# Kernel optimization log

Hardware: AMD Instinct MI355X
Metric: run time of the kernel (lower is better)

The kernel has to match this reference:

```python
import jax, jax.numpy as jnp
import numpy as np

NEG_INF = -1e9  # finite stand-in for torch's masked_fill(-inf); grad-safe


def setup_inputs() -> dict:
    key = jax.random.key(0)
    k1, k2, k3, k4, k5 = jax.random.split(key, 5)
    B, T, S, Dq, Dk = 8, 2048, 4096, 128, 128
    query = jax.random.normal(k1, (B, T, Dq), dtype=jnp.float32)
    memory_bank = jax.random.normal(k2, (B, S, Dk), dtype=jnp.float32)
    # lengths in [1, S] so every row has at least one valid source position
    memory_lengths = jax.random.randint(k3, (B,), 1, S + 1, dtype=jnp.int64)
    # nn.Linear weights: linear_in [Dk, Dq], linear_out [Dq, Dq+Dk]
    W_in = jax.random.normal(k4, (Dk, Dq), dtype=jnp.float32) / np.sqrt(Dq)
    W_out = jax.random.normal(k5, (Dq, Dq + Dk), dtype=jnp.float32) / np.sqrt(Dq + Dk)
    return {"query": query, "memory_bank": memory_bank,
            "memory_lengths": memory_lengths, "W_in": W_in, "W_out": W_out}


def reference(query, memory_bank, memory_lengths, W_in, W_out):
    B, T, Dq = query.shape
    S = memory_bank.shape[1]
    # score: project query then bmm with sources -> [B, T, S]
    h_t = jnp.einsum('btq,kq->btk', query, W_in)
    align = jnp.einsum('btk,bsk->bts', h_t, memory_bank)
    # mask invalid source positions
    valid = jnp.arange(S) < memory_lengths[:, None]            # [B, S]
    align = jnp.where(valid[:, None, :], align, NEG_INF)       # [B, T, S]
    align_vectors = jax.nn.softmax(align, axis=-1)
    # context and output projection
    c = jnp.einsum('bts,bsk->btk', align_vectors, memory_bank)  # [B, T, Dk]
    concat_c = jnp.concatenate([c, query], axis=-1)             # [B, T, Dk+Dq]
    attn_h = jnp.tanh(jnp.einsum('btc,qc->btq', concat_c, W_out))
    return attn_h, align_vectors, align
```

## Files before the change

kernel.cpp:

```cpp
#include <hip/hip_runtime.h>

#define B_ 8
#define T_ 2048
#define S_ 4096
#define D_ 128
#define N_ (B_*T_)
#define NTILE_ (S_/128)
#define NEG_INF_ (-1e9f)

__device__ __forceinline__ int load_len(const int* __restrict__ p, int b) {
    return (p[1] == 0) ? p[2*b] : p[b];
}

template<bool MASK>
__global__ __launch_bounds__(256) void gemm_nt_k128(
    const float* __restrict__ A, const float* __restrict__ Bmat,
    float* __restrict__ C, const int ldc, const long long bStride,
    const int* __restrict__ mlen,
    float* __restrict__ pmax, float* __restrict__ psum)
{
    __shared__ float At[16][128];
    __shared__ float Bt[16][128];
    const int t  = threadIdx.x;
    const int tx = t & 15, ty = t >> 4;
    const int col0 = blockIdx.x << 7;
    const int n0   = blockIdx.y << 7;
    const int b    = blockIdx.y >> 4;
    const float* Bb = Bmat + (long long)b * bStride;
    const int r_ld = t >> 1, kf = t & 1;

    float acc[8][8];
#pragma unroll
    for (int i = 0; i < 8; ++i)
#pragma unroll
        for (int j = 0; j < 8; ++j) acc[i][j] = 0.f;

    const float* Arow = &A[(long long)(n0 + r_ld) * 128];
    const float* Brow = &Bb[(long long)(col0 + r_ld) * 128];

    for (int k0 = 0; k0 < 128; k0 += 16) {
        __syncthreads();
#pragma unroll
        for (int u = 0; u < 2; ++u) {
            const int kk = kf*8 + u*4;
            const float4 va = *(const float4*)&Arow[k0 + kk];
            At[kk+0][r_ld] = va.x; At[kk+1][r_ld] = va.y;
            At[kk+2][r_ld] = va.z; At[kk+3][r_ld] = va.w;
            const float4 vb = *(const float4*)&Brow[k0 + kk];
            Bt[kk+0][r_ld] = vb.x; Bt[kk+1][r_ld] = vb.y;
            Bt[kk+2][r_ld] = vb.z; Bt[kk+3][r_ld] = vb.w;
        }
        __syncthreads();
#pragma unroll
        for (int kk = 0; kk < 16; ++kk) {
            float a[8], bv[8];
#pragma unroll
            for (int u = 0; u < 2; ++u) {
                const float4 v = *(const float4*)&At[kk][ty*8 + u*4];
                a[u*4+0]=v.x; a[u*4+1]=v.y; a[u*4+2]=v.z; a[u*4+3]=v.w;
                const float4 w = *(const float4*)&Bt[kk][tx*4 + u*64];
                bv[u*4+0]=w.x; bv[u*4+1]=w.y; bv[u*4+2]=w.z; bv[u*4+3]=w.w;
            }
#pragma unroll
            for (int i = 0; i < 8; ++i)
#pragma unroll
                for (int j = 0; j < 8; ++j)
                    acc[i][j] = fmaf(a[i], bv[j], acc[i][j]);
        }
    }

    if (MASK) {
        const int len = load_len(mlen, b);
#pragma unroll
        for (int i = 0; i < 8; ++i) {
            const int row = n0 + ty*8 + i;
            float* Crow = &C[(long long)row * ldc + col0];
            float m = -3.4e38f;
#pragma unroll
            for (int j = 0; j < 8; ++j) {
                const int cl = tx*4 + (j&3) + ((j>>2)<<6);
                float v = acc[i][j];
                if (col0 + cl >= len) v = NEG_INF_;
                acc[i][j] = v;
                m = fmaxf(m, v);
            }
            float4 w0, w1;
            w0.x=acc[i][0]; w0.y=acc[i][1]; w0.z=acc[i][2]; w0.w=acc[i][3];
            w1.x=acc[i][4]; w1.y=acc[i][5]; w1.z=acc[i][6]; w1.w=acc[i][7];
            *(float4*)&Crow[tx*4]      = w0;
            *(float4*)&Crow[tx*4 + 64] = w1;
#pragma unroll
            for (int off = 1; off < 16; off <<= 1) m = fmaxf(m, __shfl_xor(m, off, 64));
            float s = 0.f;
#pragma unroll
            for (int j = 0; j < 8; ++j) s += __expf(acc[i][j] - m);
#pragma unroll
            for (int off = 1; off < 16; off <<= 1) s += __shfl_xor(s, off, 64);
            if (tx == 0) {
                pmax[(long long)blockIdx.x * N_ + row] = m;
                psum[(long long)blockIdx.x * N_ + row] = s;
            }
        }
    } else {
#pragma unroll
        for (int i = 0; i < 8; ++i) {
            float* Crow = &C[(long long)(n0 + ty*8 + i) * ldc + col0];
            float4 w0, w1;
            w0.x=acc[i][0]; w0.y=acc[i][1]; w0.z=acc[i][2]; w0.w=acc[i][3];
            w1.x=acc[i][4]; w1.y=acc[i][5]; w1.z=acc[i][6]; w1.w=acc[i][7];
            *(float4*)&Crow[tx*4]      = w0;
            *(float4*)&Crow[tx*4 + 64] = w1;
        }
    }
}

__global__ __launch_bounds__(256) void merge_stats(
    const float* __restrict__ pmax, const float* __restrict__ psum,
    float* __restrict__ rmax, float* __restrict__ rrinv)
{
    const int r = blockIdx.x * 256 + threadIdx.x;
    float pm[NTILE_];
    float M = -3.4e38f;
#pragma unroll
    for (int i = 0; i < NTILE_; ++i) {
        pm[i] = pmax[(long long)i * N_ + r];
        M = fmaxf(M, pm[i]);
    }
    float S = 0.f;
#pragma unroll
    for (int i = 0; i < NTILE_; ++i)
        S += psum[(long long)i * N_ + r] * __expf(pm[i] - M);
    rmax[r]  = M;
    rrinv[r] = 1.0f / S;
}

__global__ __launch_bounds__(256) void av_cpart(
    const float* __restrict__ al, const float* __restrict__ mb,
    const float* __restrict__ rmax, const float* __restrict__ rrinv,
    float* __restrict__ av, float* __restrict__ cpart, const int sChunks)
{
    __shared__ float Pl[32][132];
    __shared__ float Ml[32][132];
    const int n0 = blockIdx.y << 7;
    const int b  = blockIdx.y >> 4;
    const int t  = threadIdx.x;
    const int tx = t & 15, ty = t >> 4;
    const int r_ld = t >> 1, sf = t & 1;
    const int s_m  = t >> 3, kq8 = t & 7;

    const float mM = rmax[n0 + r_ld];
    const float rR = rrinv[n0 + r_ld];

    float acc[8][8];
#pragma unroll
    for (int i = 0; i < 8; ++i)
#pragma unroll
        for (int j = 0; j < 8; ++j) acc[i][j] = 0.f;

    const int ch0 = blockIdx.x * sChunks;
    for (int ch = 0; ch < sChunks; ++ch) {
        const int s0 = (ch0 + ch) << 5;
        __syncthreads();
#pragma unroll
        for (int f = 0; f < 4; ++f) {
            const int sl = sf*16 + f*4;
            const long long g = (long long)(n0 + r_ld) * S_ + s0 + sl;
            const float4 vv = *(const float4*)&al[g];
            float4 p;
            p.x = __expf(vv.x - mM) * rR;
            p.y = __expf(vv.y - mM) * rR;
            p.z = __expf(vv.z - mM) * rR;
            p.w = __expf(vv.w - mM) * rR;
            *(float4*)&av[g] = p;
            Pl[sl+0][r_ld] = p.x; Pl[sl+1][r_ld] = p.y;
            Pl[sl+2][r_ld] = p.z; Pl[sl+3][r_ld] = p.w;
        }
#pragma unroll
        for (int f = 0; f < 4; ++f) {
            const int k = kq8*16 + f*4;
            *(float4*)&Ml[s_m][k] =
                *(const float4*)&mb[((long long)b*S_ + s0 + s_m)*128 + k];
        }
        __syncthreads();
#pragma unroll 2
        for (int s = 0; s < 32; ++s) {
            float a[8], bv[8];
#pragma unroll
            for (int u = 0; u < 2; ++u) {
                const float4 v = *(const float4*)&Pl[s][ty*8 + u*4];
                a[u*4+0]=v.x; a[u*4+1]=v.y; a[u*4+2]=v.z; a[u*4+3]=v.w;
                const float4 w = *(const float4*)&Ml[s][tx*4 + u*64];
                bv[u*4+0]=w.x; bv[u*4+1]=w.y; bv[u*4+2]=w.z; bv[u*4+3]=w.w;
            }
#pragma unroll
            for (int i = 0; i < 8; ++i)
#pragma unroll
                for (int j = 0; j < 8; ++j)
                    acc[i][j] = fmaf(a[i], bv[j], acc[i][j]);
        }
    }

    float* cp = cpart + (long long)blockIdx.x * N_ * 128;
#pragma unroll
    for (int i = 0; i < 8; ++i) {
        const long long ro = (long long)(n0 + ty*8 + i) * 128;
        float4 w0, w1;
        w0.x=acc[i][0]; w0.y=acc[i][1]; w0.z=acc[i][2]; w0.w=acc[i][3];
        w1.x=acc[i][4]; w1.y=acc[i][5]; w1.z=acc[i][6]; w1.w=acc[i][7];
        *(float4*)&cp[ro + tx*4]      = w0;
        *(float4*)&cp[ro + tx*4 + 64] = w1;
    }
}

__global__ __launch_bounds__(256) void combine_proj(
    const float* __restrict__ cpart, const int nSplit,
    const float* __restrict__ query, const float* __restrict__ Wout,
    float* __restrict__ attn)
{
    __shared__ float Cl[32][132];
    __shared__ float Ql[32][132];
    const int n0 = blockIdx.x << 5;
    const int t = threadIdx.x;
    const int r = t >> 3, kq = t & 7;
#pragma unroll
    for (int f = 0; f < 4; ++f) {
        const int k = kq*16 + f*4;
        const long long idx = (long long)(n0 + r) * 128 + k;
        float4 s4 = *(const float4*)&cpart[idx];
        for (int p = 1; p < nSplit; ++p) {
            const float4 v = *(const float4*)&cpart[(long long)p * N_ * 128 + idx];
            s4.x += v.x; s4.y += v.y; s4.z += v.z; s4.w += v.w;
        }
        *(float4*)&Cl[r][k] = s4;
        *(float4*)&Ql[r][k] = *(const float4*)&query[idx];
    }
    __syncthreads();

    const int j = t & 127, rh = t >> 7;
    float acc2[16];
#pragma unroll
    for (int rr = 0; rr < 16; ++rr) acc2[rr] = 0.f;
    const float4* Wrow = (const float4*)&Wout[j * 256];

    for (int k4 = 0; k4 < 32; ++k4) {
        const float4 w = Wrow[k4];
#pragma unroll
        for (int rr = 0; rr < 16; ++rr) {
            const float4 c4 = *(const float4*)&Cl[rh*16 + rr][k4*4];
            acc2[rr] = fmaf(c4.x, w.x, fmaf(c4.y, w.y, fmaf(c4.z, w.z, fmaf(c4.w, w.w, acc2[rr]))));
        }
    }
    for (int k4 = 0; k4 < 32; ++k4) {
        const float4 w = Wrow[32 + k4];
#pragma unroll
        for (int rr = 0; rr < 16; ++rr) {
            const float4 q4 = *(const float4*)&Ql[rh*16 + rr][k4*4];
            acc2[rr] = fmaf(q4.x, w.x, fmaf(q4.y, w.y, fmaf(q4.z, w.z, fmaf(q4.w, w.w, acc2[rr]))));
        }
    }
#pragma unroll
    for (int rr = 0; rr < 16; ++rr)
        attn[(long long)(n0 + rh*16 + rr) * 128 + j] = tanhf(acc2[rr]);
}

extern "C" void kernel_launch(void* const* d_in, const int* in_sizes, int n_in,
                              void* d_out, int out_size, void* d_ws, size_t ws_size,
                              hipStream_t stream)
{
    const float* query = (const float*)d_in[0];
    const float* mb    = (const float*)d_in[1];
    const int*   mlen  = (const int*)d_in[2];
    const float* Win   = (const float*)d_in[3];
    const float* Wout  = (const float*)d_in[4];

    float* attn  = (float*)d_out;
    float* av    = attn + (size_t)N_ * D_;
    float* align = av   + (size_t)N_ * S_;

    const size_t statsB = (size_t)2 * N_ * 4;
    const size_t partB  = (size_t)2 * NTILE_ * N_ * 4;
    const size_t matB   = (size_t)N_ * D_ * 4;

    int split = 0;
    if      (ws_size >= statsB + partB + matB + 8*matB) split = 8;
    else if (ws_size >= statsB + partB + matB + 4*matB) split = 4;
    else if (ws_size >= statsB + partB + matB + 2*matB) split = 2;
    else if (ws_size >= statsB + partB + matB + 1*matB) split = 1;

    char* w = (char*)d_ws;
    float* rmax  = (float*)w;
    float* rrinv = rmax + N_;
    float *pmax, *psum, *cpart, *ht;
    int nSplit;
    if (split > 0) {
        pmax  = (float*)(w + statsB);
        psum  = pmax + (size_t)NTILE_ * N_;
        cpart = (float*)(w + statsB + partB);
        ht    = cpart + (size_t)split * N_ * D_;
        nSplit = split;
    } else {
        pmax  = av;
        psum  = av + (size_t)NTILE_ * N_;
        ht    = av + (size_t)2 * NTILE_ * N_;
        cpart = attn;
        nSplit = 1;
    }

    gemm_nt_k128<false><<<dim3(1, 128), 256, 0, stream>>>(
        query, Win, ht, 128, 0LL, nullptr, nullptr, nullptr);
    gemm_nt_k128<true><<<dim3(S_/128, 128), 256, 0, stream>>>(
        ht, mb, align, S_, (long long)S_ * D_, mlen, pmax, psum);
    merge_stats<<<N_/256, 256, 0, stream>>>(pmax, psum, rmax, rrinv);
    av_cpart<<<dim3(nSplit, 128), 256, 0, stream>>>(
        align, mb, rmax, rrinv, av, cpart, (S_/32) / nSplit);
    combine_proj<<<N_/32, 256, 0, stream>>>(cpart, nSplit, query, Wout, attn);
}
```

Baseline: 965.9 us.

## Use split-bf16 MFMA for score and context GEMMs with masked-tile skipping

Replaces the FP32 SIMT GEMMs for align and context with bf16 MFMA kernels. Each FP32 operand is split into hi and lo bf16 parts and three MFMAs are issued per product to keep near-FP32 accuracy. It adds preprocessing kernels that split and transpose memory_bank and h_t, and it skips compute for tiles and chunks beyond memory_lengths by writing the mask or zero values directly. The cost is extra workspace and conversion traffic, plus a small precision change from dropping the lo*lo term.

```diff
diff --git a/kernel.cpp b/kernel.cpp
--- a/kernel.cpp
+++ b/kernel.cpp
@@ -8,25 +8,76 @@
 #define NTILE_ (S_/128)
 #define NEG_INF_ (-1e9f)
 
+typedef __attribute__((ext_vector_type(8))) short bf16x8;
+typedef __attribute__((ext_vector_type(4))) float f32x4;
+
 __device__ __forceinline__ int load_len(const int* __restrict__ p, int b) {
     return (p[1] == 0) ? p[2*b] : p[b];
 }
 
-template<bool MASK>
-__global__ __launch_bounds__(256) void gemm_nt_k128(
+__device__ __forceinline__ unsigned short f2bf(float x) {
+    unsigned u = __float_as_uint(x);
+    unsigned r = (u + 0x7fffu + ((u >> 16) & 1u)) >> 16;
+    return (unsigned short)r;
+}
+__device__ __forceinline__ float bf2f(unsigned short h) {
+    return __uint_as_float(((unsigned)h) << 16);
+}
+__device__ __forceinline__ unsigned pk2(unsigned short a, unsigned short b) {
+    return (unsigned)a | ((unsigned)b << 16);
+}
+
+__global__ __launch_bounds__(256) void prep_mb(
+    const float* __restrict__ mb,
+    unsigned short* __restrict__ mbh, unsigned short* __restrict__ mbl,
+    unsigned short* __restrict__ mbth, unsigned short* __restrict__ mbtl)
+{
+    __shared__ float tile[64][65];
+    const int b = blockIdx.z, f0 = blockIdx.y << 6, s0 = blockIdx.x << 6;
+    const int t = threadIdx.x;
+#pragma unroll
+    for (int i = 0; i < 4; ++i) {
+        const int c = t + (i << 8);
+        const int s = c >> 4, q = c & 15;
+        const long long ga = ((long long)(b*S_ + s0 + s)) * 128 + f0 + q*4;
+        const float4 v = *(const float4*)&mb[ga];
+        tile[s][q*4+0] = v.x; tile[s][q*4+1] = v.y;
+        tile[s][q*4+2] = v.z; tile[s][q*4+3] = v.w;
+        unsigned short h0=f2bf(v.x), h1=f2bf(v.y), h2=f2bf(v.z), h3=f2bf(v.w);
+        uint2 ph; ph.x = pk2(h0,h1); ph.y = pk2(h2,h3);
+        *(uint2*)&mbh[ga] = ph;
+        uint2 pl; pl.x = pk2(f2bf(v.x - bf2f(h0)), f2bf(v.y - bf2f(h1)));
+        pl.y = pk2(f2bf(v.z - bf2f(h2)), f2bf(v.w - bf2f(h3)));
+        *(uint2*)&mbl[ga] = pl;
+    }
+    __syncthreads();
+    const int f = t >> 2, q = t & 3;
+    unsigned short h[16], l[16];
+#pragma unroll
+    for (int ss = 0; ss < 16; ++ss) {
+        const float v = tile[q*16 + ss][f];
+        h[ss] = f2bf(v);
+        l[ss] = f2bf(v - bf2f(h[ss]));
+    }
+    const long long go = ((long long)(b*128 + f0 + f)) * S_ + s0 + q*16;
+    uint4 w0, w1;
+    w0.x=pk2(h[0],h[1]);  w0.y=pk2(h[2],h[3]);  w0.z=pk2(h[4],h[5]);  w0.w=pk2(h[6],h[7]);
+    w1.x=pk2(h[8],h[9]);  w1.y=pk2(h[10],h[11]);w1.z=pk2(h[12],h[13]);w1.w=pk2(h[14],h[15]);
+    *(uint4*)&mbth[go] = w0; *(uint4*)&mbth[go+8] = w1;
+    w0.x=pk2(l[0],l[1]);  w0.y=pk2(l[2],l[3]);  w0.z=pk2(l[4],l[5]);  w0.w=pk2(l[6],l[7]);
+    w1.x=pk2(l[8],l[9]);  w1.y=pk2(l[10],l[11]);w1.z=pk2(l[12],l[13]);w1.w=pk2(l[14],l[15]);
+    *(uint4*)&mbtl[go] = w0; *(uint4*)&mbtl[go+8] = w1;
+}
+
+__global__ __launch_bounds__(256) void ht_gemm(
     const float* __restrict__ A, const float* __restrict__ Bmat,
-    float* __restrict__ C, const int ldc, const long long bStride,
-    const int* __restrict__ mlen,
-    float* __restrict__ pmax, float* __restrict__ psum)
+    float* __restrict__ C)
 {
     __shared__ float At[16][128];
     __shared__ float Bt[16][128];
     const int t  = threadIdx.x;
     const int tx = t & 15, ty = t >> 4;
-    const int col0 = blockIdx.x << 7;
-    const int n0   = blockIdx.y << 7;
-    const int b    = blockIdx.y >> 4;
-    const float* Bb = Bmat + (long long)b * bStride;
+    const int n0 = blockIdx.y << 7;
     const int r_ld = t >> 1, kf = t & 1;
 
     float acc[8][8];
@@ -36,7 +87,7 @@
         for (int j = 0; j < 8; ++j) acc[i][j] = 0.f;
 
     const float* Arow = &A[(long long)(n0 + r_ld) * 128];
-    const float* Brow = &Bb[(long long)(col0 + r_ld) * 128];
+    const float* Brow = &Bmat[(long long)r_ld * 128];
 
     for (int k0 = 0; k0 < 128; k0 += 16) {
         __syncthreads();
@@ -68,49 +119,155 @@
                     acc[i][j] = fmaf(a[i], bv[j], acc[i][j]);
         }
     }
-
-    if (MASK) {
-        const int len = load_len(mlen, b);
-#pragma unroll
-        for (int i = 0; i < 8; ++i) {
-            const int row = n0 + ty*8 + i;
-            float* Crow = &C[(long long)row * ldc + col0];
-            float m = -3.4e38f;
-#pragma unroll
-            for (int j = 0; j < 8; ++j) {
-                const int cl = tx*4 + (j&3) + ((j>>2)<<6);
-                float v = acc[i][j];
-                if (col0 + cl >= len) v = NEG_INF_;
-                acc[i][j] = v;
-                m = fmaxf(m, v);
+#pragma unroll
+    for (int i = 0; i < 8; ++i) {
+        float* Crow = &C[(long long)(n0 + ty*8 + i) * 128];
+        float4 w0, w1;
+        w0.x=acc[i][0]; w0.y=acc[i][1]; w0.z=acc[i][2]; w0.w=acc[i][3];
+        w1.x=acc[i][4]; w1.y=acc[i][5]; w1.z=acc[i][6]; w1.w=acc[i][7];
+        *(float4*)&Crow[tx*4]      = w0;
+        *(float4*)&Crow[tx*4 + 64] = w1;
+    }
+}
+
+__global__ __launch_bounds__(256) void split_bf16(
+    const float* __restrict__ in, unsigned short* __restrict__ hi,
+    unsigned short* __restrict__ lo, int n4)
+{
+    const int i = blockIdx.x * 256 + threadIdx.x;
+    if (i >= n4) return;
+    const float4 v = *(const float4*)&in[i*4];
+    unsigned short h0=f2bf(v.x), h1=f2bf(v.y), h2=f2bf(v.z), h3=f2bf(v.w);
+    uint2 ph; ph.x = pk2(h0,h1); ph.y = pk2(h2,h3);
+    *(uint2*)&hi[i*4] = ph;
+    uint2 pl; pl.x = pk2(f2bf(v.x-bf2f(h0)), f2bf(v.y-bf2f(h1)));
+    pl.y = pk2(f2bf(v.z-bf2f(h2)), f2bf(v.w-bf2f(h3)));
+    *(uint2*)&lo[i*4] = pl;
+}
+
+__global__ __launch_bounds__(256) void qk_mfma(
+    const unsigned short* __restrict__ hth, const unsigned short* __restrict__ htl,
+    const unsigned short* __restrict__ mbh, const unsigned short* __restrict__ mbl,
+    float* __restrict__ alignO, const int* __restrict__ mlen,
+    float* __restrict__ pmax, float* __restrict__ psum)
+{
+    __shared__ __align__(16) unsigned short Ah[128*40], Al[128*40];
+    __shared__ __align__(16) unsigned short Bh[128*40], Bl[128*40];
+    __shared__ float sm[2][128], ss[2][128];
+    const int t = threadIdx.x, l = t & 63, w = t >> 6;
+    const int wm = w >> 1, wn = w & 1, g = l >> 4, lr = l & 15;
+    const int c0 = blockIdx.x << 7, n0 = blockIdx.y << 7;
+    const int b  = blockIdx.y >> 4;
+    const int len = load_len(mlen, b);
+
+    if (c0 >= len) {
+        const int r = t >> 1, half = (t & 1) << 6;
+        float4 neg; neg.x = neg.y = neg.z = neg.w = NEG_INF_;
+        float* Crow = &alignO[(long long)(n0 + r) * S_ + c0 + half];
+#pragma unroll
+        for (int q = 0; q < 16; ++q) *(float4*)&Crow[q*4] = neg;
+        if (t < 128) {
+            pmax[(long long)blockIdx.x * N_ + n0 + t] = NEG_INF_;
+            psum[(long long)blockIdx.x * N_ + n0 + t] = 128.f;
+        }
+        return;
+    }
+
+    f32x4 acc[4][4];
+#pragma unroll
+    for (int mt = 0; mt < 4; ++mt)
+#pragma unroll
+        for (int nt = 0; nt < 4; ++nt) acc[mt][nt] = (f32x4)0.f;
+
+    for (int k0 = 0; k0 < 128; k0 += 32) {
+        __syncthreads();
+#pragma unroll
+        for (int i = 0; i < 2; ++i) {
+            const int c = t + (i << 8);
+            const int row = c >> 2, sl = c & 3;
+            const int go = (n0 + row)*128 + k0 + sl*8;
+            *(uint4*)&Ah[row*40 + sl*8] = *(const uint4*)&hth[go];
+            *(uint4*)&Al[row*40 + sl*8] = *(const uint4*)&htl[go];
+            const long long gb = ((long long)b*S_ + c0 + row)*128 + k0 + sl*8;
+            *(uint4*)&Bh[row*40 + sl*8] = *(const uint4*)&mbh[gb];
+            *(uint4*)&Bl[row*40 + sl*8] = *(const uint4*)&mbl[gb];
+        }
+        __syncthreads();
+        bf16x8 ah[4], al[4];
+#pragma unroll
+        for (int mt = 0; mt < 4; ++mt) {
+            const int r = wm*64 + mt*16 + lr;
+            ah[mt] = *(const bf16x8*)&Ah[r*40 + g*8];
+            al[mt] = *(const bf16x8*)&Al[r*40 + g*8];
+        }
+#pragma unroll
+        for (int nt = 0; nt < 4; ++nt) {
+            const int cc = wn*64 + nt*16 + lr;
+            const bf16x8 bh = *(const bf16x8*)&Bh[cc*40 + g*8];
+            const bf16x8 bl = *(const bf16x8*)&Bl[cc*40 + g*8];
+#pragma unroll
+            for (int mt = 0; mt < 4; ++mt) {
+                acc[mt][nt] = __builtin_amdgcn_mfma_f32_16x16x32_bf16(ah[mt], bh, acc[mt][nt], 0, 0, 0);
+                acc[mt][nt] = __builtin_amdgcn_mfma_f32_16x16x32_bf16(ah[mt], bl, acc[mt][nt], 0, 0, 0);
+                acc[mt][nt] = __builtin_amdgcn_mfma_f32_16x16x32_bf16(al[mt], bh, acc[mt][nt], 0, 0, 0);
             }
-            float4 w0, w1;
-            w0.x=acc[i][0]; w0.y=acc[i][1]; w0.z=acc[i][2]; w0.w=acc[i][3];
-            w1.x=acc[i][4]; w1.y=acc[i][5]; w1.z=acc[i][6]; w1.w=acc[i][7];
-            *(float4*)&Crow[tx*4]      = w0;
-            *(float4*)&Crow[tx*4 + 64] = w1;
-#pragma unroll
-            for (int off = 1; off < 16; off <<= 1) m = fmaxf(m, __shfl_xor(m, off, 64));
-            float s = 0.f;
-#pragma unroll
-            for (int j = 0; j < 8; ++j) s += __expf(acc[i][j] - m);
-#pragma unroll
-            for (int off = 1; off < 16; off <<= 1) s += __shfl_xor(s, off, 64);
-            if (tx == 0) {
-                pmax[(long long)blockIdx.x * N_ + row] = m;
-                psum[(long long)blockIdx.x * N_ + row] = s;
+        }
+    }
+
+#pragma unroll
+    for (int nt = 0; nt < 4; ++nt) {
+        const int col = c0 + wn*64 + nt*16 + lr;
+        if (col >= len) {
+#pragma unroll
+            for (int mt = 0; mt < 4; ++mt)
+#pragma unroll
+                for (int j = 0; j < 4; ++j) acc[mt][nt][j] = NEG_INF_;
+        }
+    }
+#pragma unroll
+    for (int mt = 0; mt < 4; ++mt) {
+        float m[4] = {-3.4e38f, -3.4e38f, -3.4e38f, -3.4e38f};
+#pragma unroll
+        for (int nt = 0; nt < 4; ++nt)
+#pragma unroll
+            for (int j = 0; j < 4; ++j) m[j] = fmaxf(m[j], acc[mt][nt][j]);
+#pragma unroll
+        for (int j = 0; j < 4; ++j)
+#pragma unroll
+            for (int off = 1; off < 16; off <<= 1)
+                m[j] = fmaxf(m[j], __shfl_xor(m[j], off, 64));
+        float s[4] = {0.f, 0.f, 0.f, 0.f};
+#pragma unroll
+        for (int nt = 0; nt < 4; ++nt)
+#pragma unroll
+            for (int j = 0; j < 4; ++j) s[j] += __expf(acc[mt][nt][j] - m[j]);
+#pragma unroll
+        for (int j = 0; j < 4; ++j)
+#pragma unroll
+            for (int off = 1; off < 16; off <<= 1)
+                s[j] += __shfl_xor(s[j], off, 64);
+        if (lr == 0) {
+#pragma unroll
+            for (int j = 0; j < 4; ++j) {
+                const int row = wm*64 + mt*16 + 4*g + j;
+                sm[wn][row] = m[j]; ss[wn][row] = s[j];
             }
         }
-    } else {
-#pragma unroll
-        for (int i = 0; i < 8; ++i) {
-            float* Crow = &C[(long long)(n0 + ty*8 + i) * ldc + col0];
-            float4 w0, w1;
-            w0.x=acc[i][0]; w0.y=acc[i][1]; w0.z=acc[i][2]; w0.w=acc[i][3];
-            w1.x=acc[i][4]; w1.y=acc[i][5]; w1.z=acc[i][6]; w1.w=acc[i][7];
-            *(float4*)&Crow[tx*4]      = w0;
-            *(float4*)&Crow[tx*4 + 64] = w1;
-        }
+#pragma unroll
+        for (int nt = 0; nt < 4; ++nt) {
+            const int col = c0 + wn*64 + nt*16 + lr;
+#pragma unroll
+            for (int j = 0; j < 4; ++j)
+                alignO[(long long)(n0 + wm*64 + mt*16 + 4*g + j)*S_ + col] = acc[mt][nt][j];
+        }
+    }
+    __syncthreads();
+    if (t < 128) {
+        const float m0 = sm[0][t], m1 = sm[1][t];
+        const float M = fmaxf(m0, m1);
+        const float Sv = ss[0][t]*__expf(m0 - M) + ss[1][t]*__expf(m1 - M);
+        pmax[(long long)blockIdx.x * N_ + n0 + t] = M;
+        psum[(long long)blockIdx.x * N_ + n0 + t] = Sv;
     }
 }
 
@@ -134,82 +291,103 @@
     rrinv[r] = 1.0f / S;
 }
 
-__global__ __launch_bounds__(256) void av_cpart(
-    const float* __restrict__ al, const float* __restrict__ mb,
+__global__ __launch_bounds__(256) void pv_mfma(
+    const float* __restrict__ alignI,
+    const unsigned short* __restrict__ mbth, const unsigned short* __restrict__ mbtl,
     const float* __restrict__ rmax, const float* __restrict__ rrinv,
+    const int* __restrict__ mlen,
     float* __restrict__ av, float* __restrict__ cpart, const int sChunks)
 {
-    __shared__ float Pl[32][132];
-    __shared__ float Ml[32][132];
-    const int n0 = blockIdx.y << 7;
-    const int b  = blockIdx.y >> 4;
-    const int t  = threadIdx.x;
-    const int tx = t & 15, ty = t >> 4;
-    const int r_ld = t >> 1, sf = t & 1;
-    const int s_m  = t >> 3, kq8 = t & 7;
-
-    const float mM = rmax[n0 + r_ld];
-    const float rR = rrinv[n0 + r_ld];
-
-    float acc[8][8];
-#pragma unroll
-    for (int i = 0; i < 8; ++i)
-#pragma unroll
-        for (int j = 0; j < 8; ++j) acc[i][j] = 0.f;
-
-    const int ch0 = blockIdx.x * sChunks;
+    __shared__ __align__(16) unsigned short Ph[128*40], Pl[128*40];
+    __shared__ __align__(16) unsigned short Vh[128*40], Vl[128*40];
+    const int t = threadIdx.x, l = t & 63, w = t >> 6;
+    const int wm = w >> 1, wn = w & 1, g = l >> 4, lr = l & 15;
+    const int n0 = blockIdx.y << 7, b = blockIdx.y >> 4;
+    const int r_st = t >> 1, hf = t & 1;
+    const int len = load_len(mlen, b);
+    const float M = rmax[n0 + r_st], R = rrinv[n0 + r_st];
+
+    f32x4 acc[4][4];
+#pragma unroll
+    for (int mt = 0; mt < 4; ++mt)
+#pragma unroll
+        for (int nt = 0; nt < 4; ++nt) acc[mt][nt] = (f32x4)0.f;
+
+    const int s00 = blockIdx.x * sChunks * 32;
     for (int ch = 0; ch < sChunks; ++ch) {
-        const int s0 = (ch0 + ch) << 5;
-        __syncthreads();
-#pragma unroll
-        for (int f = 0; f < 4; ++f) {
-            const int sl = sf*16 + f*4;
-            const long long g = (long long)(n0 + r_ld) * S_ + s0 + sl;
-            const float4 vv = *(const float4*)&al[g];
-            float4 p;
-            p.x = __expf(vv.x - mM) * rR;
-            p.y = __expf(vv.y - mM) * rR;
-            p.z = __expf(vv.z - mM) * rR;
-            p.w = __expf(vv.w - mM) * rR;
-            *(float4*)&av[g] = p;
-            Pl[sl+0][r_ld] = p.x; Pl[sl+1][r_ld] = p.y;
-            Pl[sl+2][r_ld] = p.z; Pl[sl+3][r_ld] = p.w;
-        }
-#pragma unroll
-        for (int f = 0; f < 4; ++f) {
-            const int k = kq8*16 + f*4;
-            *(float4*)&Ml[s_m][k] =
-                *(const float4*)&mb[((long long)b*S_ + s0 + s_m)*128 + k];
-        }
-        __syncthreads();
-#pragma unroll 2
-        for (int s = 0; s < 32; ++s) {
-            float a[8], bv[8];
-#pragma unroll
-            for (int u = 0; u < 2; ++u) {
-                const float4 v = *(const float4*)&Pl[s][ty*8 + u*4];
-                a[u*4+0]=v.x; a[u*4+1]=v.y; a[u*4+2]=v.z; a[u*4+3]=v.w;
-                const float4 w = *(const float4*)&Ml[s][tx*4 + u*64];
-                bv[u*4+0]=w.x; bv[u*4+1]=w.y; bv[u*4+2]=w.z; bv[u*4+3]=w.w;
+        const int s0 = s00 + (ch << 5);
+        if (s0 >= len) {
+            const long long ga = (long long)(n0 + r_st)*S_ + s0 + hf*16;
+            float4 z; z.x = z.y = z.z = z.w = 0.f;
+#pragma unroll
+            for (int q = 0; q < 4; ++q) *(float4*)&av[ga + q*4] = z;
+            continue;
+        }
+        __syncthreads();
+        {
+            unsigned short ph[16], pl[16];
+            const long long ga = (long long)(n0 + r_st)*S_ + s0 + hf*16;
+#pragma unroll
+            for (int q = 0; q < 4; ++q) {
+                const float4 v = *(const float4*)&alignI[ga + q*4];
+                float4 p;
+                p.x = __expf(v.x - M)*R; p.y = __expf(v.y - M)*R;
+                p.z = __expf(v.z - M)*R; p.w = __expf(v.w - M)*R;
+                *(float4*)&av[ga + q*4] = p;
+                ph[q*4+0]=f2bf(p.x); pl[q*4+0]=f2bf(p.x - bf2f(ph[q*4+0]));
+                ph[q*4+1]=f2bf(p.y); pl[q*4+1]=f2bf(p.y - bf2f(ph[q*4+1]));
+                ph[q*4+2]=f2bf(p.z); pl[q*4+2]=f2bf(p.z - bf2f(ph[q*4+2]));
+                ph[q*4+3]=f2bf(p.w); pl[q*4+3]=f2bf(p.w - bf2f(ph[q*4+3]));
             }
-#pragma unroll
-            for (int i = 0; i < 8; ++i)
-#pragma unroll
-                for (int j = 0; j < 8; ++j)
-                    acc[i][j] = fmaf(a[i], bv[j], acc[i][j]);
+            uint4 w0, w1;
+            w0.x=pk2(ph[0],ph[1]);  w0.y=pk2(ph[2],ph[3]);  w0.z=pk2(ph[4],ph[5]);  w0.w=pk2(ph[6],ph[7]);
+            w1.x=pk2(ph[8],ph[9]);  w1.y=pk2(ph[10],ph[11]);w1.z=pk2(ph[12],ph[13]);w1.w=pk2(ph[14],ph[15]);
+            *(uint4*)&Ph[r_st*40 + hf*16]     = w0;
+            *(uint4*)&Ph[r_st*40 + hf*16 + 8] = w1;
+            w0.x=pk2(pl[0],pl[1]);  w0.y=pk2(pl[2],pl[3]);  w0.z=pk2(pl[4],pl[5]);  w0.w=pk2(pl[6],pl[7]);
+            w1.x=pk2(pl[8],pl[9]);  w1.y=pk2(pl[10],pl[11]);w1.z=pk2(pl[12],pl[13]);w1.w=pk2(pl[14],pl[15]);
+            *(uint4*)&Pl[r_st*40 + hf*16]     = w0;
+            *(uint4*)&Pl[r_st*40 + hf*16 + 8] = w1;
+        }
+#pragma unroll
+        for (int i = 0; i < 2; ++i) {
+            const int c = t + (i << 8);
+            const int f = c >> 2, sl = c & 3;
+            const long long gv = ((long long)(b*128 + f))*S_ + s0 + sl*8;
+            *(uint4*)&Vh[f*40 + sl*8] = *(const uint4*)&mbth[gv];
+            *(uint4*)&Vl[f*40 + sl*8] = *(const uint4*)&mbtl[gv];
+        }
+        __syncthreads();
+        bf16x8 ph[4], pl[4];
+#pragma unroll
+        for (int mt = 0; mt < 4; ++mt) {
+            const int r = wm*64 + mt*16 + lr;
+            ph[mt] = *(const bf16x8*)&Ph[r*40 + g*8];
+            pl[mt] = *(const bf16x8*)&Pl[r*40 + g*8];
+        }
+#pragma unroll
+        for (int nt = 0; nt < 4; ++nt) {
+            const int f = wn*64 + nt*16 + lr;
+            const bf16x8 vh = *(const bf16x8*)&Vh[f*40 + g*8];
+            const bf16x8 vl = *(const bf16x8*)&Vl[f*40 + g*8];
+#pragma unroll
+            for (int mt = 0; mt < 4; ++mt) {
+                acc[mt][nt] = __builtin_amdgcn_mfma_f32_16x16x32_bf16(ph[mt], vh, acc[mt][nt], 0, 0, 0);
+                acc[mt][nt] = __builtin_amdgcn_mfma_f32_16x16x32_bf16(ph[mt], vl, acc[mt][nt], 0, 0, 0);
+                acc[mt][nt] = __builtin_amdgcn_mfma_f32_16x16x32_bf16(pl[mt], vh, acc[mt][nt], 0, 0, 0);
+            }
         }
     }
 
     float* cp = cpart + (long long)blockIdx.x * N_ * 128;
 #pragma unroll
-    for (int i = 0; i < 8; ++i) {
-        const long long ro = (long long)(n0 + ty*8 + i) * 128;
-        float4 w0, w1;
-        w0.x=acc[i][0]; w0.y=acc[i][1]; w0.z=acc[i][2]; w0.w=acc[i][3];
-        w1.x=acc[i][4]; w1.y=acc[i][5]; w1.z=acc[i][6]; w1.w=acc[i][7];
-        *(float4*)&cp[ro + tx*4]      = w0;
-        *(float4*)&cp[ro + tx*4 + 64] = w1;
-    }
+    for (int mt = 0; mt < 4; ++mt)
+#pragma unroll
+        for (int nt = 0; nt < 4; ++nt)
+#pragma unroll
+            for (int j = 0; j < 4; ++j)
+                cp[(long long)(n0 + wm*64 + mt*16 + 4*g + j)*128 + wn*64 + nt*16 + lr]
+                    = acc[mt][nt][j];
 }
 
 __global__ __launch_bounds__(256) void combine_proj(
@@ -277,41 +455,35 @@
     float* av    = attn + (size_t)N_ * D_;
     float* align = av   + (size_t)N_ * S_;
 
-    const size_t statsB = (size_t)2 * N_ * 4;
-    const size_t partB  = (size_t)2 * NTILE_ * N_ * 4;
-    const size_t matB   = (size_t)N_ * D_ * 4;
-
-    int split = 0;
-    if      (ws_size >= statsB + partB + matB + 8*matB) split = 8;
-    else if (ws_size >= statsB + partB + matB + 4*matB) split = 4;
-    else if (ws_size >= statsB + partB + matB + 2*matB) split = 2;
-    else if (ws_size >= statsB + partB + matB + 1*matB) split = 1;
-
-    char* w = (char*)d_ws;
-    float* rmax  = (float*)w;
-    float* rrinv = rmax + N_;
-    float *pmax, *psum, *cpart, *ht;
-    int nSplit;
-    if (split > 0) {
-        pmax  = (float*)(w + statsB);
-        psum  = pmax + (size_t)NTILE_ * N_;
-        cpart = (float*)(w + statsB + partB);
-        ht    = cpart + (size_t)split * N_ * D_;
-        nSplit = split;
-    } else {
-        pmax  = av;
-        psum  = av + (size_t)NTILE_ * N_;
-        ht    = av + (size_t)2 * NTILE_ * N_;
-        cpart = attn;
-        nSplit = 1;
-    }
-
-    gemm_nt_k128<false><<<dim3(1, 128), 256, 0, stream>>>(
-        query, Win, ht, 128, 0LL, nullptr, nullptr, nullptr);
-    gemm_nt_k128<true><<<dim3(S_/128, 128), 256, 0, stream>>>(
-        ht, mb, align, S_, (long long)S_ * D_, mlen, pmax, psum);
+    char* p = (char*)d_ws;
+    float* rmax  = (float*)p;                 p += (size_t)N_ * 4;
+    float* rrinv = (float*)p;                 p += (size_t)N_ * 4;
+    float* pmax  = (float*)p;                 p += (size_t)NTILE_ * N_ * 4;
+    float* psum  = (float*)p;                 p += (size_t)NTILE_ * N_ * 4;
+    float* ht    = (float*)p;                 p += (size_t)N_ * D_ * 4;
+    unsigned short* hth  = (unsigned short*)p; p += (size_t)N_ * D_ * 2;
+    unsigned short* htl  = (unsigned short*)p; p += (size_t)N_ * D_ * 2;
+    unsigned short* mbh  = (unsigned short*)p; p += (size_t)B_ * S_ * D_ * 2;
+    unsigned short* mbl  = (unsigned short*)p; p += (size_t)B_ * S_ * D_ * 2;
+    unsigned short* mbth = (unsigned short*)p; p += (size_t)B_ * S_ * D_ * 2;
+    unsigned short* mbtl = (unsigned short*)p; p += (size_t)B_ * S_ * D_ * 2;
+    const size_t usedBase = (size_t)(p - (char*)d_ws);
+    const size_t matB = (size_t)N_ * D_ * 4;
+
+    int split;
+    float* cpart;
+    if (ws_size >= usedBase + 4*matB)      { split = 4; cpart = (float*)p; }
+    else if (ws_size >= usedBase + 2*matB) { split = 2; cpart = (float*)p; }
+    else if (ws_size >= usedBase + matB)   { split = 1; cpart = (float*)p; }
+    else                                   { split = 1; cpart = attn; }
+
+    prep_mb<<<dim3(S_/64, 2, B_), 256, 0, stream>>>(mb, mbh, mbl, mbth, mbtl);
+    ht_gemm<<<dim3(1, N_/128), 256, 0, stream>>>(query, Win, ht);
+    split_bf16<<<(N_*D_/4)/256, 256, 0, stream>>>(ht, hth, htl, N_*D_/4);
+    qk_mfma<<<dim3(S_/128, N_/128), 256, 0, stream>>>(
+        hth, htl, mbh, mbl, align, mlen, pmax, psum);
     merge_stats<<<N_/256, 256, 0, stream>>>(pmax, psum, rmax, rrinv);
-    av_cpart<<<dim3(nSplit, 128), 256, 0, stream>>>(
-        align, mb, rmax, rrinv, av, cpart, (S_/32) / nSplit);
-    combine_proj<<<N_/32, 256, 0, stream>>>(cpart, nSplit, query, Wout, attn);
-}
+    pv_mfma<<<dim3(split, N_/128), 256, 0, stream>>>(
+        align, mbth, mbtl, rmax, rrinv, mlen, av, cpart, (S_/32)/split);
+    combine_proj<<<N_/32, 256, 0, stream>>>(cpart, split, query, Wout, attn);
+}
```

Result: faster. 808.6 us (-16.3%).
